# Optimization experiments

Measured on AMD Instinct MI355X. Metric: run time of the kernel, lower is better.

The kernel has to match this reference:

```python
import jax, jax.numpy as jnp
import numpy as np

N = 50_000          # nodes
E = 1_600_000       # edges (avg degree 32)
IN = 128            # in_feats
H = 4               # num_heads
F = 32              # out_feats per head
CUTOFF = 4.0        # bessel_cutoff
P = 7               # envelope_exponent + 1
ENV_A = -(P + 1) * (P + 2) / 2.0   # -36
ENV_B = P * (P + 2)                # 63
ENV_C = -P * (P + 1) / 2.0         # -28


def setup_inputs() -> dict:
    key = jax.random.key(0)
    ks = jax.random.split(key, 8)
    x = jax.random.normal(ks[0], (N, IN), dtype=jnp.float32)
    distance = jax.random.uniform(ks[1], (E,), dtype=jnp.float32) * CUTOFF
    W_src = jax.random.normal(ks[2], (H * F, IN), dtype=jnp.float32) * 0.05
    b_src = jnp.zeros((H * F,), dtype=jnp.float32)
    W_dst = jax.random.normal(ks[3], (H * F, IN), dtype=jnp.float32) * 0.05
    b_dst = jnp.zeros((H * F,), dtype=jnp.float32)
    attn = jax.random.normal(ks[4], (1, H, F), dtype=jnp.float32) * 0.1
    prelu_alpha = jnp.full((H,), 0.25, dtype=jnp.float32)
    frequencies = jnp.arange(1.0, H + 1.0, dtype=jnp.float32) * np.pi
    src = jax.random.randint(ks[5], (E,), 0, N, dtype=jnp.int32)
    dst = jax.random.randint(ks[6], (E,), 0, N, dtype=jnp.int32)
    return dict(x=x, distance=distance, W_src=W_src, b_src=b_src,
                W_dst=W_dst, b_dst=b_dst, attn=attn,
                prelu_alpha=prelu_alpha, frequencies=frequencies,
                src=src, dst=dst)


def _bessel_coeff(distance, frequencies):
    # distance: [E] -> d_scaled: [E,1]; frequencies: [H] -> coeff: [E,H]
    d = (distance / CUTOFF)[:, None]
    d_p0 = d ** P
    env = d + ENV_A * d_p0 + ENV_B * (d_p0 * d) + ENV_C * (d_p0 * d * d)
    return env * jnp.sin(frequencies * d)


def reference(x, distance, W_src, b_src, W_dst, b_dst, attn,
              prelu_alpha, frequencies, src, dst):
    n = x.shape[0]
    feat_src = (x @ W_src.T + b_src).reshape(n, H, F)   # [N,H,F]
    feat_dst = (x @ W_dst.T + b_dst).reshape(n, H, F)   # [N,H,F]

    coeff = _bessel_coeff(distance, frequencies)[:, :, None]  # [E,H,1]

    el = feat_src[src]                                  # [E,H,F] gather
    e = (el + feat_dst[dst]) * coeff                    # u_add_v then bessel scale
    e = jnp.where(e >= 0, e, prelu_alpha[None, :, None] * e)  # PReLU per head
    score = jnp.einsum('ehf,hf->eh', e, attn[0])        # [E,H]

    # edge softmax over incoming edges per dst node, per head
    seg_max = jax.ops.segment_max(score, dst, num_segments=n)        # [N,H]
    ex = jnp.exp(score - seg_max[dst])                               # [E,H]
    denom = jax.ops.segment_sum(ex, dst, num_segments=n)             # [N,H]
    a = ex / denom[dst]                                              # [E,H]

    # u_mul_e + scatter-sum aggregation
    msgs = el * a[:, :, None]                                        # [E,H,F]
    rst = jax.ops.segment_sum(msgs, dst, num_segments=n)             # [N,H,F]
    return rst
```

## Files before the change

### kernel.cpp

```cpp
#include <hip/hip_runtime.h>
#include <hip/hip_bf16.h>
#include <math.h>

#define N_NODES 50000
#define E_EDGES 1600000
#define HF 128
#define INV_CUTOFF 0.25f
#define ENV_A -36.0f
#define ENV_B 63.0f
#define ENV_C -28.0f

#define GEMM_BLOCKS ((N_NODES + 63) / 64)
#define REC_CAP 72
#define NBUCK 196
#define BUCK_CAP 8960
#define EPB 6250

typedef __attribute__((ext_vector_type(8))) short bf16x8;
typedef __attribute__((ext_vector_type(4))) float f32x4;

__device__ __forceinline__ unsigned short f2bf(float f) {
  unsigned u = __float_as_uint(f);
  u += 0x7fffu + ((u >> 16) & 1u);
  return (unsigned short)(u >> 16);
}
__device__ __forceinline__ unsigned pack2(float lo, float hi) {
  return (unsigned)f2bf(lo) | ((unsigned)f2bf(hi) << 16);
}
__device__ __forceinline__ float2 up2(unsigned v) {
  return make_float2(__uint_as_float(v << 16), __uint_as_float(v & 0xffff0000u));
}
__device__ __forceinline__ float2 pk_fma(float2 a, float2 b, float2 c) {
  return make_float2(fmaf(a.x, b.x, c.x), fmaf(a.y, b.y, c.y));
}
__device__ __forceinline__ float2 pk_add(float2 a, float2 b) {
  return make_float2(a.x + b.x, a.y + b.y);
}
__device__ __forceinline__ float2 pk_max0(float2 a) {
  return make_float2(fmaxf(a.x, 0.f), fmaxf(a.y, 0.f));
}
__device__ __forceinline__ float2 pk_min0(float2 a) {
  return make_float2(fminf(a.x, 0.f), fminf(a.y, 0.f));
}

__global__ void prep_w(const float* __restrict__ Ws, const float* __restrict__ Wd,
                       unsigned short* __restrict__ wbf) {
  const int q = blockIdx.x * 256 + threadIdx.x;
  if (q < 4096) {
    const int n = q >> 4, c = q & 15;
    const float* Wp = ((n < 128) ? Ws : Wd) + (size_t)(n & 127) * HF + c * 8;
    const float4 v0 = *(const float4*)Wp;
    const float4 v1 = *(const float4*)(Wp + 4);
    uint4 pk;
    pk.x = pack2(v0.x, v0.y); pk.y = pack2(v0.z, v0.w);
    pk.z = pack2(v1.x, v1.y); pk.w = pack2(v1.z, v1.w);
    *(uint4*)(wbf + (size_t)n * HF + ((c ^ (n & 15)) * 8)) = pk;
  }
}

__global__ __launch_bounds__(256) void feat_gemm(
    const float* __restrict__ x, const unsigned short* __restrict__ wbf,
    const float* __restrict__ bs, const float* __restrict__ bd,
    unsigned short* __restrict__ fs, float* __restrict__ fd) {
  __shared__ unsigned short wlds[256 * 128];

  for (int i = threadIdx.x; i < 4096; i += 256)
    ((uint4*)wlds)[i] = ((const uint4*)wbf)[i];

  const int lane = threadIdx.x & 63;
  const int wave = threadIdx.x >> 6;
  const int m = lane & 15;
  const int quad = lane >> 4;
  const int m0 = blockIdx.x * 64 + wave * 16;
  const int row = m0 + m;
  const int rowc = (row < N_NODES) ? row : (N_NODES - 1);

  union { bf16x8 v; unsigned u[4]; } af[4];
  #pragma unroll
  for (int kt = 0; kt < 4; kt++) {
    const float* xp = x + (size_t)rowc * HF + kt * 32 + quad * 8;
    const float4 u0 = *(const float4*)xp;
    const float4 u1 = *(const float4*)(xp + 4);
    af[kt].u[0] = pack2(u0.x, u0.y); af[kt].u[1] = pack2(u0.z, u0.w);
    af[kt].u[2] = pack2(u1.x, u1.y); af[kt].u[3] = pack2(u1.z, u1.w);
  }

  __syncthreads();

  float accA[16][4];
  #pragma unroll
  for (int nt = 0; nt < 16; nt++) {
    const int nrow = nt * 16 + m;
    f32x4 acc = {0.f, 0.f, 0.f, 0.f};
    #pragma unroll
    for (int kt = 0; kt < 4; kt++) {
      const int pc = (kt * 4 + quad) ^ m;
      const bf16x8 bf = *(const bf16x8*)(wlds + (size_t)nrow * HF + pc * 8);
      acc = __builtin_amdgcn_mfma_f32_16x16x32_bf16(af[kt].v, bf, acc, 0, 0, 0);
    }
    accA[nt][0] = acc[0]; accA[nt][1] = acc[1];
    accA[nt][2] = acc[2]; accA[nt][3] = acc[3];
  }

  __syncthreads();
  unsigned short* fsS = wlds;
  float* fdS = (float*)(wlds + 64 * 136);

  const int rl0 = wave * 16 + quad * 4;
  #pragma unroll
  for (int nt = 0; nt < 16; nt++) {
    const int col = nt * 16 + m;
    if (col < 128) {
      const float bias = bs[col];
      #pragma unroll
      for (int r = 0; r < 4; r++)
        fsS[(rl0 + r) * 136 + col] = f2bf(accA[nt][r] + bias);
    } else {
      const float bias = bd[col - 128];
      #pragma unroll
      for (int r = 0; r < 4; r++)
        fdS[(rl0 + r) * 132 + (col - 128)] = accA[nt][r] + bias;
    }
  }
  __syncthreads();

  for (int c = threadIdx.x; c < 1024; c += 256) {
    const int r = c >> 4, off = (c & 15) * 8;
    const int gr = blockIdx.x * 64 + r;
    if (gr < N_NODES)
      *(uint4*)(fs + (size_t)gr * HF + off) = *(const uint4*)(fsS + r * 136 + off);
  }
  for (int c = threadIdx.x; c < 2048; c += 256) {
    const int r = c >> 5, off = (c & 31) * 4;
    const int gr = blockIdx.x * 64 + r;
    if (gr < N_NODES)
      *(float4*)(fd + (size_t)gr * HF + off) = *(const float4*)(fdS + r * 132 + off);
  }
}

__global__ __launch_bounds__(256) void bucketize(
    const int* __restrict__ dst, const int* __restrict__ src,
    const float* __restrict__ dist,
    int* __restrict__ bcursor, unsigned* __restrict__ bb_pay,
    unsigned char* __restrict__ bb_loc) {
  __shared__ unsigned pay_s[EPB];
  __shared__ unsigned char bkt_s[EPB];
  __shared__ unsigned char loc_s[EPB];
  __shared__ int hist[NBUCK], loff[NBUCK], base[NBUCK], cur[NBUCK];
  for (int t = threadIdx.x; t < NBUCK; t += 256) { hist[t] = 0; cur[t] = 0; }
  __syncthreads();
  const int lo = blockIdx.x * EPB;
  for (int k = threadIdx.x; k < EPB; k += 256)
    atomicAdd(&hist[dst[lo + k] >> 8], 1);
  __syncthreads();
  if (threadIdx.x == 0) {
    int run = 0;
    for (int j = 0; j < NBUCK; j++) { loff[j] = run; run += hist[j]; }
  }
  __syncthreads();
  for (int t = threadIdx.x; t < NBUCK; t += 256)
    base[t] = atomicAdd(&bcursor[t], hist[t]);
  __syncthreads();
  for (int k = threadIdx.x; k < EPB; k += 256) {
    const int d = dst[lo + k];
    const int b = d >> 8;
    float ds = dist[lo + k] * (INV_CUTOFF * 65536.f);
    unsigned dq = (unsigned)(ds + 0.5f);
    if (dq > 65535u) dq = 65535u;
    const int s = loff[b] + atomicAdd(&cur[b], 1);
    pay_s[s] = (unsigned)src[lo + k] | (dq << 16);
    bkt_s[s] = (unsigned char)b;
    loc_s[s] = (unsigned char)(d & 255);
  }
  __syncthreads();
  for (int s = threadIdx.x; s < EPB; s += 256) {
    const int b = bkt_s[s];
    const int dest = base[b] + (s - loff[b]);
    if (dest < BUCK_CAP) {
      bb_pay[(size_t)b * BUCK_CAP + dest] = pay_s[s];
      bb_loc[(size_t)b * BUCK_CAP + dest] = loc_s[s];
    }
  }
}

__global__ __launch_bounds__(256) void bucket_scatter(
    const int* __restrict__ bcursor, const unsigned* __restrict__ bb_pay,
    const unsigned char* __restrict__ bb_loc,
    int* __restrict__ counts, unsigned* __restrict__ rec) {
  __shared__ int cnt[256];
  __shared__ unsigned recS[256 * REC_CAP];
  cnt[threadIdx.x] = 0;
  __syncthreads();
  const int b = blockIdx.x;
  const int total = min(bcursor[b], BUCK_CAP);
  const size_t base = (size_t)b * BUCK_CAP;
  for (int i = threadIdx.x; i < total; i += 256) {
    const unsigned pay = bb_pay[base + i];
    const int local = bb_loc[base + i];
    const int r = atomicAdd(&cnt[local], 1);
    if (r < REC_CAP) recS[local * REC_CAP + r] = pay;
  }
  __syncthreads();
  const int node0 = b << 8;
  uint4* dstp = (uint4*)(rec + (size_t)node0 * REC_CAP);
  const uint4* srcp = (const uint4*)recS;
  for (int i = threadIdx.x; i < 256 * REC_CAP / 4; i += 256)
    dstp[i] = srcp[i];
  const int node = node0 + (int)threadIdx.x;
  if (node < N_NODES) counts[node] = min(cnt[threadIdx.x], REC_CAP);
}

__global__ __launch_bounds__(256) void gat_agg(
    const unsigned short* __restrict__ fs, const float* __restrict__ fd,
    const int* __restrict__ counts, const unsigned* __restrict__ rec,
    const float* __restrict__ attn, const float* __restrict__ alpha_p,
    const float* __restrict__ freqs, float* __restrict__ out) {
  const int wave = threadIdx.x >> 6;
  const int lane = threadIdx.x & 63;
  const int node = blockIdx.x * 4 + wave;
  if (node >= N_NODES) return;
  const int eslot = lane >> 4;
  const int h = (lane >> 2) & 3;
  const int j = lane & 3;
  const int fo = (h << 5) + (j << 3);

  const float* fdp = fd + (size_t)node * HF + fo;
  const float2 f0 = *(const float2*)(fdp + 0);
  const float2 f1 = *(const float2*)(fdp + 2);
  const float2 f2 = *(const float2*)(fdp + 4);
  const float2 f3 = *(const float2*)(fdp + 6);
  const float2 t0 = *(const float2*)(attn + fo + 0);
  const float2 t1 = *(const float2*)(attn + fo + 2);
  const float2 t2 = *(const float2*)(attn + fo + 4);
  const float2 t3 = *(const float2*)(attn + fo + 6);
  const float al = alpha_p[h];
  const float fr = freqs[h];

  const int beg = node * REC_CAP;
  int cnt = counts[node];
  cnt = (cnt < REC_CAP) ? cnt : REC_CAP;
  const int end = beg + cnt;

  float l = 0.f;
  float2 A0 = {0.f, 0.f}, A1 = {0.f, 0.f}, A2 = {0.f, 0.f}, A3 = {0.f, 0.f};

  for (int i = beg; i < end; i += 4) {
    const int e = i + eslot;
    const bool valid = (e < end);
    const unsigned r = rec[valid ? e : beg];
    const int s_idx = (int)(r & 0xffffu);
    const float d = (float)(r >> 16) * (1.0f / 65536.0f);
    const uint4 eb = *(const uint4*)(fs + (size_t)s_idx * HF + fo);
    const float2 e0 = up2(eb.x);
    const float2 e1 = up2(eb.y);
    const float2 e2 = up2(eb.z);
    const float2 e3 = up2(eb.w);

    const float d2 = d * d;
    const float d4 = d2 * d2;
    const float d7 = d4 * d2 * d;
    const float env = fmaf(d7, fmaf(d, fmaf(d, ENV_C, ENV_B), ENV_A), d);
    const float cf = env * __sinf(fr * d);
    const float acf = al * cf;
    const float cpos = (cf >= 0.f) ? cf : acf;
    const float cneg = (cf >= 0.f) ? acf : cf;

    float2 sp = {0.f, 0.f}, sn = {0.f, 0.f};
    float2 u;
    u = pk_add(e0, f0); sp = pk_fma(pk_max0(u), t0, sp); sn = pk_fma(pk_min0(u), t0, sn);
    u = pk_add(e1, f1); sp = pk_fma(pk_max0(u), t1, sp); sn = pk_fma(pk_min0(u), t1, sn);
    u = pk_add(e2, f2); sp = pk_fma(pk_max0(u), t2, sp); sn = pk_fma(pk_min0(u), t2, sn);
    u = pk_add(e3, f3); sp = pk_fma(pk_max0(u), t3, sp); sn = pk_fma(pk_min0(u), t3, sn);
    float p = fmaf(cpos, sp.x + sp.y, cneg * (sn.x + sn.y));

    p += __shfl_xor(p, 1);
    p += __shfl_xor(p, 2);

    const float w = valid ? __expf(p) : 0.f;
    l += w;
    const float2 w2 = {w, w};
    A0 = pk_fma(w2, e0, A0);
    A1 = pk_fma(w2, e1, A1);
    A2 = pk_fma(w2, e2, A2);
    A3 = pk_fma(w2, e3, A3);
  }

  #pragma unroll
  for (int mm = 16; mm < 64; mm <<= 1) {
    l    += __shfl_xor(l, mm);
    A0.x += __shfl_xor(A0.x, mm); A0.y += __shfl_xor(A0.y, mm);
    A1.x += __shfl_xor(A1.x, mm); A1.y += __shfl_xor(A1.y, mm);
    A2.x += __shfl_xor(A2.x, mm); A2.y += __shfl_xor(A2.y, mm);
    A3.x += __shfl_xor(A3.x, mm); A3.y += __shfl_xor(A3.y, mm);
  }

  if (eslot == 0) {
    const float rl = (l > 0.f) ? 1.0f / l : 0.f;
    float* o = out + (size_t)node * HF + fo;
    float4 o0 = {A0.x * rl, A0.y * rl, A1.x * rl, A1.y * rl};
    float4 o1 = {A2.x * rl, A2.y * rl, A3.x * rl, A3.y * rl};
    *(float4*)o = o0;
    *(float4*)(o + 4) = o1;
  }
}

extern "C" void kernel_launch(void* const* d_in, const int* in_sizes, int n_in,
                              void* d_out, int out_size, void* d_ws, size_t ws_size,
                              hipStream_t stream) {
  const float* x      = (const float*)d_in[0];
  const float* dist   = (const float*)d_in[1];
  const float* W_src  = (const float*)d_in[2];
  const float* b_src  = (const float*)d_in[3];
  const float* W_dst  = (const float*)d_in[4];
  const float* b_dst  = (const float*)d_in[5];
  const float* attn   = (const float*)d_in[6];
  const float* alpha  = (const float*)d_in[7];
  const float* freqs  = (const float*)d_in[8];
  const int*   src    = (const int*)d_in[9];
  const int*   dst    = (const int*)d_in[10];
  float* out = (float*)d_out;

  char* w = (char*)d_ws;
  size_t off = 0;
  auto alloc = [&](size_t bytes) -> void* {
    void* p = w + off;
    off += (bytes + 255) & ~(size_t)255;
    return p;
  };
  unsigned short* feat_src = (unsigned short*)alloc((size_t)N_NODES * HF * 2);
  float*          feat_dst = (float*)alloc((size_t)N_NODES * HF * 4);
  unsigned short* wbf      = (unsigned short*)alloc((size_t)256 * HF * 2);
  int*            counts   = (int*)alloc((size_t)N_NODES * 4);
  int*            bcursor  = (int*)alloc((size_t)NBUCK * 4);
  unsigned*       bb_pay   = (unsigned*)alloc((size_t)NBUCK * BUCK_CAP * 4);
  unsigned char*  bb_loc   = (unsigned char*)alloc((size_t)NBUCK * BUCK_CAP);
  unsigned*       rec      = (unsigned*)alloc((size_t)NBUCK * 256 * REC_CAP * 4);

  hipMemsetAsync(bcursor, 0, (size_t)NBUCK * 4, stream);

  prep_w<<<16, 256, 0, stream>>>(W_src, W_dst, wbf);

  feat_gemm<<<GEMM_BLOCKS, 256, 0, stream>>>(x, wbf, b_src, b_dst, feat_src, feat_dst);

  bucketize<<<256, 256, 0, stream>>>(dst, src, dist, bcursor, bb_pay, bb_loc);

  bucket_scatter<<<NBUCK, 256, 0, stream>>>(bcursor, bb_pay, bb_loc, counts, rec);

  gat_agg<<<(N_NODES + 3) / 4, 256, 0, stream>>>(
      feat_src, feat_dst, counts, rec, attn, alpha, freqs, out);
}
```

Before: 253.0 us.

## Replace two-pass bucket sort with direct atomic edge scatter; simplify PReLU scoring

Drops the two-stage bucketize/bucket_scatter pipeline and replaces it with one kernel that appends each edge directly into its destination node's fixed-capacity record slot using global atomics. The count array is now zeroed inside prep_w, which removes the memset and the intermediate bucket buffers. The PReLU score is rewritten algebraically as c1*cf*dot(u,t) + c2*|cf|*dot(|u|,t), and the packed add/fma are emitted as inline v_pk_* assembly. The cost is heavy global atomic contention and scattered 4-byte writes in place of coalesced LDS-staged writes, and the order of records within each node becomes nondeterministic.

```diff
diff --git a/kernel.cpp b/kernel.cpp
--- a/kernel.cpp
+++ b/kernel.cpp
@@ -12,9 +12,6 @@
 
 #define GEMM_BLOCKS ((N_NODES + 63) / 64)
 #define REC_CAP 72
-#define NBUCK 196
-#define BUCK_CAP 8960
-#define EPB 6250
 
 typedef __attribute__((ext_vector_type(8))) short bf16x8;
 typedef __attribute__((ext_vector_type(4))) float f32x4;
@@ -30,21 +27,27 @@
 __device__ __forceinline__ float2 up2(unsigned v) {
   return make_float2(__uint_as_float(v << 16), __uint_as_float(v & 0xffff0000u));
 }
+
+__device__ __forceinline__ float2 pk_add(float2 a, float2 b) {
+  float2 d;
+  asm("v_pk_add_f32 %0, %1, %2" : "=v"(d) : "v"(a), "v"(b));
+  return d;
+}
 __device__ __forceinline__ float2 pk_fma(float2 a, float2 b, float2 c) {
-  return make_float2(fmaf(a.x, b.x, c.x), fmaf(a.y, b.y, c.y));
-}
-__device__ __forceinline__ float2 pk_add(float2 a, float2 b) {
-  return make_float2(a.x + b.x, a.y + b.y);
-}
-__device__ __forceinline__ float2 pk_max0(float2 a) {
-  return make_float2(fmaxf(a.x, 0.f), fmaxf(a.y, 0.f));
-}
-__device__ __forceinline__ float2 pk_min0(float2 a) {
-  return make_float2(fminf(a.x, 0.f), fminf(a.y, 0.f));
-}
-
-__global__ void prep_w(const float* __restrict__ Ws, const float* __restrict__ Wd,
-                       unsigned short* __restrict__ wbf) {
+  float2 d;
+  asm("v_pk_fma_f32 %0, %1, %2, %3" : "=v"(d) : "v"(a), "v"(b), "v"(c));
+  return d;
+}
+__device__ __forceinline__ float2 pk_abs(float2 a) {
+  float2 d;
+  d.x = __uint_as_float(__float_as_uint(a.x) & 0x7fffffffu);
+  d.y = __uint_as_float(__float_as_uint(a.y) & 0x7fffffffu);
+  return d;
+}
+
+__global__ __launch_bounds__(256) void prep_w(
+    const float* __restrict__ Ws, const float* __restrict__ Wd,
+    unsigned short* __restrict__ wbf, int* __restrict__ counts) {
   const int q = blockIdx.x * 256 + threadIdx.x;
   if (q < 4096) {
     const int n = q >> 4, c = q & 15;
@@ -56,6 +59,7 @@
     pk.z = pack2(v1.x, v1.y); pk.w = pack2(v1.z, v1.w);
     *(uint4*)(wbf + (size_t)n * HF + ((c ^ (n & 15)) * 8)) = pk;
   }
+  if (q < N_NODES) counts[q] = 0;
 }
 
 __global__ __launch_bounds__(256) void feat_gemm(
@@ -138,76 +142,19 @@
   }
 }
 
-__global__ __launch_bounds__(256) void bucketize(
+__global__ __launch_bounds__(256) void edge_scatter(
     const int* __restrict__ dst, const int* __restrict__ src,
     const float* __restrict__ dist,
-    int* __restrict__ bcursor, unsigned* __restrict__ bb_pay,
-    unsigned char* __restrict__ bb_loc) {
-  __shared__ unsigned pay_s[EPB];
-  __shared__ unsigned char bkt_s[EPB];
-  __shared__ unsigned char loc_s[EPB];
-  __shared__ int hist[NBUCK], loff[NBUCK], base[NBUCK], cur[NBUCK];
-  for (int t = threadIdx.x; t < NBUCK; t += 256) { hist[t] = 0; cur[t] = 0; }
-  __syncthreads();
-  const int lo = blockIdx.x * EPB;
-  for (int k = threadIdx.x; k < EPB; k += 256)
-    atomicAdd(&hist[dst[lo + k] >> 8], 1);
-  __syncthreads();
-  if (threadIdx.x == 0) {
-    int run = 0;
-    for (int j = 0; j < NBUCK; j++) { loff[j] = run; run += hist[j]; }
-  }
-  __syncthreads();
-  for (int t = threadIdx.x; t < NBUCK; t += 256)
-    base[t] = atomicAdd(&bcursor[t], hist[t]);
-  __syncthreads();
-  for (int k = threadIdx.x; k < EPB; k += 256) {
-    const int d = dst[lo + k];
-    const int b = d >> 8;
-    float ds = dist[lo + k] * (INV_CUTOFF * 65536.f);
-    unsigned dq = (unsigned)(ds + 0.5f);
-    if (dq > 65535u) dq = 65535u;
-    const int s = loff[b] + atomicAdd(&cur[b], 1);
-    pay_s[s] = (unsigned)src[lo + k] | (dq << 16);
-    bkt_s[s] = (unsigned char)b;
-    loc_s[s] = (unsigned char)(d & 255);
-  }
-  __syncthreads();
-  for (int s = threadIdx.x; s < EPB; s += 256) {
-    const int b = bkt_s[s];
-    const int dest = base[b] + (s - loff[b]);
-    if (dest < BUCK_CAP) {
-      bb_pay[(size_t)b * BUCK_CAP + dest] = pay_s[s];
-      bb_loc[(size_t)b * BUCK_CAP + dest] = loc_s[s];
-    }
-  }
-}
-
-__global__ __launch_bounds__(256) void bucket_scatter(
-    const int* __restrict__ bcursor, const unsigned* __restrict__ bb_pay,
-    const unsigned char* __restrict__ bb_loc,
     int* __restrict__ counts, unsigned* __restrict__ rec) {
-  __shared__ int cnt[256];
-  __shared__ unsigned recS[256 * REC_CAP];
-  cnt[threadIdx.x] = 0;
-  __syncthreads();
-  const int b = blockIdx.x;
-  const int total = min(bcursor[b], BUCK_CAP);
-  const size_t base = (size_t)b * BUCK_CAP;
-  for (int i = threadIdx.x; i < total; i += 256) {
-    const unsigned pay = bb_pay[base + i];
-    const int local = bb_loc[base + i];
-    const int r = atomicAdd(&cnt[local], 1);
-    if (r < REC_CAP) recS[local * REC_CAP + r] = pay;
-  }
-  __syncthreads();
-  const int node0 = b << 8;
-  uint4* dstp = (uint4*)(rec + (size_t)node0 * REC_CAP);
-  const uint4* srcp = (const uint4*)recS;
-  for (int i = threadIdx.x; i < 256 * REC_CAP / 4; i += 256)
-    dstp[i] = srcp[i];
-  const int node = node0 + (int)threadIdx.x;
-  if (node < N_NODES) counts[node] = min(cnt[threadIdx.x], REC_CAP);
+  const int i = blockIdx.x * 256 + threadIdx.x;
+  if (i >= E_EDGES) return;
+  const int d = dst[i];
+  float ds = dist[i] * (INV_CUTOFF * 65536.f);
+  unsigned dq = (unsigned)(ds + 0.5f);
+  if (dq > 65535u) dq = 65535u;
+  const unsigned pay = (unsigned)src[i] | (dq << 16);
+  const int pos = atomicAdd(&counts[d], 1);
+  if (pos < REC_CAP) rec[(size_t)d * REC_CAP + pos] = pay;
 }
 
 __global__ __launch_bounds__(256) void gat_agg(
@@ -234,6 +181,8 @@
   const float2 t2 = *(const float2*)(attn + fo + 4);
   const float2 t3 = *(const float2*)(attn + fo + 6);
   const float al = alpha_p[h];
+  const float c1 = 0.5f * (1.0f + al);
+  const float c2 = 0.5f * (1.0f - al);
   const float fr = freqs[h];
 
   const int beg = node * REC_CAP;
@@ -261,18 +210,17 @@
     const float d7 = d4 * d2 * d;
     const float env = fmaf(d7, fmaf(d, fmaf(d, ENV_C, ENV_B), ENV_A), d);
     const float cf = env * __sinf(fr * d);
-    const float acf = al * cf;
-    const float cpos = (cf >= 0.f) ? cf : acf;
-    const float cneg = (cf >= 0.f) ? acf : cf;
-
-    float2 sp = {0.f, 0.f}, sn = {0.f, 0.f};
+    const float k1 = c1 * cf;
+    const float k2 = c2 * fabsf(cf);
+
+    float2 D1 = {0.f, 0.f}, D2 = {0.f, 0.f};
     float2 u;
-    u = pk_add(e0, f0); sp = pk_fma(pk_max0(u), t0, sp); sn = pk_fma(pk_min0(u), t0, sn);
-    u = pk_add(e1, f1); sp = pk_fma(pk_max0(u), t1, sp); sn = pk_fma(pk_min0(u), t1, sn);
-    u = pk_add(e2, f2); sp = pk_fma(pk_max0(u), t2, sp); sn = pk_fma(pk_min0(u), t2, sn);
-    u = pk_add(e3, f3); sp = pk_fma(pk_max0(u), t3, sp); sn = pk_fma(pk_min0(u), t3, sn);
-    float p = fmaf(cpos, sp.x + sp.y, cneg * (sn.x + sn.y));
-
+    u = pk_add(e0, f0); D1 = pk_fma(u, t0, D1); D2 = pk_fma(pk_abs(u), t0, D2);
+    u = pk_add(e1, f1); D1 = pk_fma(u, t1, D1); D2 = pk_fma(pk_abs(u), t1, D2);
+    u = pk_add(e2, f2); D1 = pk_fma(u, t2, D1); D2 = pk_fma(pk_abs(u), t2, D2);
+    u = pk_add(e3, f3); D1 = pk_fma(u, t3, D1); D2 = pk_fma(pk_abs(u), t3, D2);
+
+    float p = fmaf(k1, D1.x + D1.y, k2 * (D2.x + D2.y));
     p += __shfl_xor(p, 1);
     p += __shfl_xor(p, 2);
 
@@ -331,20 +279,13 @@
   float*          feat_dst = (float*)alloc((size_t)N_NODES * HF * 4);
   unsigned short* wbf      = (unsigned short*)alloc((size_t)256 * HF * 2);
   int*            counts   = (int*)alloc((size_t)N_NODES * 4);
-  int*            bcursor  = (int*)alloc((size_t)NBUCK * 4);
-  unsigned*       bb_pay   = (unsigned*)alloc((size_t)NBUCK * BUCK_CAP * 4);
-  unsigned char*  bb_loc   = (unsigned char*)alloc((size_t)NBUCK * BUCK_CAP);
-  unsigned*       rec      = (unsigned*)alloc((size_t)NBUCK * 256 * REC_CAP * 4);
-
-  hipMemsetAsync(bcursor, 0, (size_t)NBUCK * 4, stream);
-
-  prep_w<<<16, 256, 0, stream>>>(W_src, W_dst, wbf);
+  unsigned*       rec      = (unsigned*)alloc((size_t)N_NODES * REC_CAP * 4);
+
+  prep_w<<<256, 256, 0, stream>>>(W_src, W_dst, wbf, counts);
 
   feat_gemm<<<GEMM_BLOCKS, 256, 0, stream>>>(x, wbf, b_src, b_dst, feat_src, feat_dst);
 
-  bucketize<<<256, 256, 0, stream>>>(dst, src, dist, bcursor, bb_pay, bb_loc);
-
-  bucket_scatter<<<NBUCK, 256, 0, stream>>>(bcursor, bb_pay, bb_loc, counts, rec);
+  edge_scatter<<<(E_EDGES + 255) / 256, 256, 0, stream>>>(dst, src, dist, counts, rec);
 
   gat_agg<<<(N_NODES + 3) / 4, 256, 0, stream>>>(
       feat_src, feat_dst, counts, rec, attn, alpha, freqs, out);
```

Result: slower. 306.6 us (+21.2%).
